# Optimization experiments

Hardware: AMD Instinct MI355X
Metric: run time of the kernel (lower is better)

## Reference

```python
import jax, jax.numpy as jnp
import numpy as np

K = 3
LAMBDA_AMP = 0.1
N_NODES = 100000
N_EDGES = 1600000
D_FEAT = 50


def _proximal_l21(x, lambda_):
    # rowwise L2,1 shrinkage: scale each row by max(||row||-lambda,0)/||row||
    row_norm = jnp.linalg.norm(x, axis=1)  # [N]
    score = jnp.maximum(row_norm - lambda_, 0.0)
    score = jnp.where(row_norm > 0, score / jnp.where(row_norm > 0, row_norm, 1.0), score)
    return score[:, None] * x


def setup_inputs() -> dict:
    key = jax.random.key(0)
    k1, k2, k3, k4 = jax.random.split(key, 4)
    feat = jax.random.normal(k1, (N_NODES, D_FEAT), dtype=jnp.float32)
    edge_weight = jax.random.uniform(k2, (N_EDGES,), dtype=jnp.float32)
    src = jax.random.randint(k3, (N_EDGES,), 0, N_NODES, dtype=jnp.int32)
    dst = jax.random.randint(k4, (N_EDGES,), 0, N_NODES, dtype=jnp.int32)
    return {"feat": feat, "edge_weight": edge_weight, "src": src, "dst": dst}


def reference(feat, edge_weight, src, dst):
    n = feat.shape[0]
    # add self-loops (add_self_loop=True), self-loop weight = 1
    loop = jnp.arange(n, dtype=src.dtype)
    src_f = jnp.concatenate([src, loop])
    dst_f = jnp.concatenate([dst, loop])
    ew = jnp.concatenate([edge_weight, jnp.ones((n,), dtype=edge_weight.dtype)])

    # norm='both': w_ji = ew / (sqrt(out_deg(j)) * sqrt(in_deg(i))), weighted degrees
    out_deg = jax.ops.segment_sum(ew, src_f, num_segments=n)
    in_deg = jax.ops.segment_sum(ew, dst_f, num_segments=n)
    inv_sqrt_out = jnp.where(out_deg > 0, out_deg, 1.0) ** -0.5 * (out_deg > 0)
    inv_sqrt_in = jnp.where(in_deg > 0, in_deg, 1.0) ** -0.5 * (in_deg > 0)
    w = ew * inv_sqrt_out[src_f] * inv_sqrt_in[dst_f]  # [E+N]

    lam = LAMBDA_AMP
    gamma = 1.0 / (2.0 * (1.0 - lam))
    hh = feat
    x = feat
    for _ in range(K):
        # compute_LX: x - A_norm x  (u_mul_e + sum == SpMM over edges)
        agg = jax.ops.segment_sum(x[src_f] * w[:, None], dst_f, num_segments=n)
        lx = x - agg
        y = x - gamma * 2.0 * (1.0 - lam) * lx
        x = hh + _proximal_l21(y - hh, gamma * lam)
    return x
```

## Files before the change

### kernel.cpp

```cpp
#include <hip/hip_runtime.h>
#include <hip/hip_bf16.h>
#include <hip/hip_fp16.h>

#define D 50
#define PADH 64
#define GLAM 0.05555555555555555f
#define SCAN_B 1024
#define FIXS 8388608.0f
#define INV_FIXS (1.0f / 8388608.0f)
#define WSC 32768.0f
#define INV_WSC (1.0f / 32768.0f)
#define EPB 4096
#define B2T 512
#define BSH 9
#define BMSK 511u
#define BT 512
#define MAXB 256
#define MAXRUN 12288
#define NXCD 8

typedef unsigned long long u64;

__global__ void k_b1p(const int* __restrict__ src, const int* __restrict__ dst,
                      int* __restrict__ mat, const float* __restrict__ feat,
                      __half* __restrict__ xp, int e, int nblk, int nbuk, int n) {
    if ((int)blockIdx.x < nblk) {
        __shared__ unsigned hd[MAXB], hs[MAXB];
        for (int j = threadIdx.x; j < nbuk; j += blockDim.x) { hd[j] = 0; hs[j] = 0; }
        __syncthreads();
        int base = blockIdx.x * EPB;
        int end = base + EPB; if (end > e) end = e;
        for (int i = base + threadIdx.x; i < end; i += blockDim.x) {
            int t = __builtin_nontemporal_load(dst + i);
            int s = __builtin_nontemporal_load(src + i);
            atomicAdd(&hd[t >> BSH], 1u);
            atomicAdd(&hs[s >> BSH], 1u);
        }
        __syncthreads();
        for (int j = threadIdx.x; j < nbuk; j += blockDim.x) {
            mat[j * nblk + blockIdx.x] = (int)hd[j];
            mat[(nbuk + j) * nblk + blockIdx.x] = (int)hs[j];
        }
    } else {
        int i = ((int)blockIdx.x - nblk) * (int)blockDim.x + (int)threadIdx.x;
        if (i < n * PADH) {
            int node = i >> 6, col = i & 63;
            xp[i] = (col < D) ? __float2half_rn(feat[node * D + col]) : __half(0.0f);
        }
    }
}

__global__ void k_scan1(const int* __restrict__ cnt, int* __restrict__ out,
                        int* __restrict__ bsum, int n) {
    __shared__ int s[SCAN_B];
    int i = blockIdx.x * SCAN_B + threadIdx.x;
    int v = (i < n) ? cnt[i] : 0;
    s[threadIdx.x] = v; __syncthreads();
    for (int off = 1; off < SCAN_B; off <<= 1) {
        int t = (threadIdx.x >= (unsigned)off) ? s[threadIdx.x - off] : 0;
        __syncthreads();
        s[threadIdx.x] += t; __syncthreads();
    }
    if (i < n) out[i] = s[threadIdx.x] - v;
    if (threadIdx.x == SCAN_B - 1) bsum[blockIdx.x] = s[threadIdx.x];
}

__global__ void k_scan2(int* __restrict__ bsum, int nb) {
    __shared__ int s[SCAN_B];
    int v = (threadIdx.x < (unsigned)nb) ? bsum[threadIdx.x] : 0;
    s[threadIdx.x] = v; __syncthreads();
    for (int off = 1; off < SCAN_B; off <<= 1) {
        int t = (threadIdx.x >= (unsigned)off) ? s[threadIdx.x - off] : 0;
        __syncthreads();
        s[threadIdx.x] += t; __syncthreads();
    }
    if (threadIdx.x < (unsigned)nb) bsum[threadIdx.x] = s[threadIdx.x] - v;
}

__global__ void k_scan3(int* __restrict__ out, const int* __restrict__ bsum, int n) {
    int i = blockIdx.x * SCAN_B + threadIdx.x;
    if (i < n) out[i] += bsum[blockIdx.x];
}

__device__ __forceinline__ int xcd_swz(int p, int nwg) {
    int q = nwg / NXCD, r = nwg % NXCD;
    int xcd = p % NXCD, idx = p / NXCD;
    return (xcd < r ? xcd * (q + 1) : r * (q + 1) + (xcd - r) * q) + idx;
}

__global__ __launch_bounds__(B2T, 4) void k_b2(
                     const float* __restrict__ ew, const int* __restrict__ src,
                     const int* __restrict__ dst, const int* __restrict__ msc,
                     u64* __restrict__ bind, unsigned* __restrict__ bins,
                     int e, int nblk, int nbuk) {
    __shared__ unsigned cd[MAXB], cs[MAXB];
    __shared__ unsigned ld[MAXB], ls[MAXB];
    __shared__ int gbd[MAXB], gbs[MAXB];
    __shared__ u64 sd[EPB];
    __shared__ unsigned ss[EPB];
    __shared__ unsigned char bdd[EPB], bds[EPB];
    int tid = threadIdx.x;
    int wb = xcd_swz((int)blockIdx.x, nblk);
    for (int j = tid; j < MAXB; j += blockDim.x) { cd[j] = 0; cs[j] = 0; }
    __syncthreads();
    int base = wb * EPB;
    int end = base + EPB; if (end > e) end = e;
    int m = end - base;

    for (int i = base + tid; i < end; i += blockDim.x) {
        atomicAdd(&cd[(unsigned)__builtin_nontemporal_load(dst + i) >> BSH], 1u);
        atomicAdd(&cs[(unsigned)__builtin_nontemporal_load(src + i) >> BSH], 1u);
    }
    __syncthreads();

    unsigned vd = 0, vs = 0;
    if (tid < MAXB) { vd = cd[tid]; vs = cs[tid]; ld[tid] = vd; ls[tid] = vs; }
    __syncthreads();
    for (int off = 1; off < MAXB; off <<= 1) {
        unsigned td = 0, ts = 0;
        if (tid < MAXB && tid >= off) { td = ld[tid - off]; ts = ls[tid - off]; }
        __syncthreads();
        if (tid < MAXB) { ld[tid] += td; ls[tid] += ts; }
        __syncthreads();
    }
    if (tid < MAXB) {
        ld[tid] -= vd; ls[tid] -= vs;
        cd[tid] = ld[tid]; cs[tid] = ls[tid];
        if (tid < nbuk) {
            gbd[tid] = msc[tid * nblk + wb];
            gbs[tid] = msc[(nbuk + tid) * nblk + wb] - e;
        }
    }
    __syncthreads();

    for (int i = base + tid; i < end; i += blockDim.x) {
        float w = __builtin_nontemporal_load(ew + i);
        int s = __builtin_nontemporal_load(src + i);
        int t = __builtin_nontemporal_load(dst + i);
        unsigned wfix = (unsigned)(w * FIXS + 0.5f);
        if (wfix > 0x7FFFFFu) wfix = 0x7FFFFFu;
        unsigned tb = (unsigned)t >> BSH, sb = (unsigned)s >> BSH;
        unsigned pd = atomicAdd(&cd[tb], 1u);
        sd[pd] = ((u64)__float_as_uint(w) << 32)
               | ((unsigned)s << BSH) | (unsigned)(t & BMSK);
        bdd[pd] = (unsigned char)tb;
        unsigned ps = atomicAdd(&cs[sb], 1u);
        ss[ps] = (wfix << BSH) | (unsigned)(s & BMSK);
        bds[ps] = (unsigned char)sb;
    }
    __syncthreads();

    for (int p = tid; p < m; p += blockDim.x) {
        unsigned jd = bdd[p];
        bind[gbd[jd] + (int)(p - ld[jd])] = sd[p];
        unsigned js = bds[p];
        bins[gbs[js] + (int)(p - ls[js])] = ss[p];
    }
}

__global__ void k_srcdeg(const unsigned* __restrict__ bins, const int* __restrict__ msc,
                         float* __restrict__ iso, int n, int nblk, int nbuk, int e) {
    __shared__ unsigned wl[BT];
    wl[threadIdx.x] = 0;
    __syncthreads();
    int b = blockIdx.x;
    int start = msc[(nbuk + b) * nblk] - e;
    int end = (b + 1 < nbuk) ? (msc[(nbuk + b + 1) * nblk] - e) : e;
    for (int i = start + threadIdx.x; i < end; i += blockDim.x) {
        unsigned r = bins[i];
        atomicAdd(&wl[r & BMSK], r >> BSH);
    }
    __syncthreads();
    int node = b * BT + threadIdx.x;
    if (node < n)
        iso[node] = rsqrtf(1.0f + (float)wl[threadIdx.x] * INV_FIXS);
}

__global__ void k_dstfill(const u64* __restrict__ bind, const int* __restrict__ msc,
                          const float* __restrict__ iso, float* __restrict__ isi,
                          int* __restrict__ cnt, int* __restrict__ rowptr,
                          unsigned* __restrict__ pe, int n, int nblk, int nbuk, int e) {
    __shared__ unsigned pst[MAXRUN];
    __shared__ unsigned cl[BT], wl[BT], cur[BT];
    __shared__ int sc[BT];
    __shared__ float isL[BT];
    cl[threadIdx.x] = 0; wl[threadIdx.x] = 0;
    __syncthreads();
    int b = blockIdx.x;
    int start = msc[b * nblk];
    int end = (b + 1 < nbuk) ? msc[(b + 1) * nblk] : e;
    int run = end - start;
    bool fast = (run <= MAXRUN);

    for (int i = start + threadIdx.x; i < end; i += blockDim.x) {
        u64 r = bind[i];
        unsigned loc = (unsigned)r & BMSK;
        float w = __uint_as_float((unsigned)(r >> 32));
        unsigned wfix = (unsigned)(w * FIXS + 0.5f);
        if (wfix > 0x7FFFFFu) wfix = 0x7FFFFFu;
        atomicAdd(&cl[loc], 1u);
        atomicAdd(&wl[loc], wfix);
    }
    __syncthreads();

    int myc = (int)cl[threadIdx.x];
    sc[threadIdx.x] = myc;
    __syncthreads();
    for (int off = 1; off < BT; off <<= 1) {
        int t = (threadIdx.x >= (unsigned)off) ? sc[threadIdx.x - off] : 0;
        __syncthreads();
        sc[threadIdx.x] += t;
        __syncthreads();
    }
    int lex = sc[threadIdx.x] - myc;
    int lrp = start + lex;

    float myisi = rsqrtf(1.0f + (float)wl[threadIdx.x] * INV_FIXS);
    isL[threadIdx.x] = myisi;
    cur[threadIdx.x] = fast ? (unsigned)lex : (unsigned)lrp;

    int node = b * BT + threadIdx.x;
    if (node < n) {
        isi[node] = myisi;
        cnt[node] = myc;
        rowptr[node] = lrp;
    }
    __syncthreads();

    if (fast) {
        for (int i = start + threadIdx.x; i < end; i += blockDim.x) {
            u64 r = bind[i];
            unsigned lo = (unsigned)r;
            unsigned tloc = lo & BMSK;
            unsigned s = lo >> BSH;
            float w = __uint_as_float((unsigned)(r >> 32));
            float wv = w * iso[s] * isL[tloc];
            unsigned wq = (unsigned)(wv * WSC + 0.5f);
            if (wq > 32767u) wq = 32767u;
            unsigned pos = atomicAdd(&cur[tloc], 1u);
            pst[pos] = (s << 15) | wq;
        }
        __syncthreads();
        for (int p = threadIdx.x; p < run; p += blockDim.x)
            pe[start + p] = pst[p];
    } else {
        for (int i = start + threadIdx.x; i < end; i += blockDim.x) {
            u64 r = bind[i];
            unsigned lo = (unsigned)r;
            unsigned tloc = lo & BMSK;
            unsigned s = lo >> BSH;
            float w = __uint_as_float((unsigned)(r >> 32));
            float wv = w * iso[s] * isL[tloc];
            unsigned wq = (unsigned)(wv * WSC + 0.5f);
            if (wq > 32767u) wq = 32767u;
            unsigned pos = atomicAdd(&cur[tloc], 1u);
            pe[pos] = (s << 15) | wq;
        }
    }
}

__device__ __forceinline__ void acc_edge(const uint4& u, float w,
                                         float& a0, float& a1, float& a2, float& a3,
                                         float& a4, float& a5, float& a6, float& a7) {
    const __half2* hp = (const __half2*)&u;
    float2 f0 = __half22float2(hp[0]);
    float2 f1 = __half22float2(hp[1]);
    float2 f2 = __half22float2(hp[2]);
    float2 f3 = __half22float2(hp[3]);
    a0 = fmaf(w, f0.x, a0); a1 = fmaf(w, f0.y, a1);
    a2 = fmaf(w, f1.x, a2); a3 = fmaf(w, f1.y, a3);
    a4 = fmaf(w, f2.x, a4); a5 = fmaf(w, f2.y, a5);
    a6 = fmaf(w, f3.x, a6); a7 = fmaf(w, f3.y, a7);
}

__global__ void k_iter(const int* __restrict__ rowptr, const int* __restrict__ cnt,
                       const unsigned* __restrict__ pe, const __half* __restrict__ xin,
                       const __half* __restrict__ xpF, const float* __restrict__ iso,
                       const float* __restrict__ isi, __half* __restrict__ hout,
                       float* __restrict__ fout, int n, int final_iter) {
    int lane = threadIdx.x & 63;
    int c    = lane & 7;
    int waveId = (blockIdx.x * blockDim.x + threadIdx.x) >> 6;
    int node = waveId * 8 + (lane >> 3);
    if (node >= n) return;

    float a0 = 0.f, a1 = 0.f, a2 = 0.f, a3 = 0.f;
    float a4 = 0.f, a5 = 0.f, a6 = 0.f, a7 = 0.f;

    int beg = rowptr[node], m = cnt[node];

    int j = 0;
    for (; j + 8 <= m; j += 8) {
        unsigned p0 = pe[beg + j];
        unsigned p1 = pe[beg + j + 1];
        unsigned p2 = pe[beg + j + 2];
        unsigned p3 = pe[beg + j + 3];
        unsigned p4 = pe[beg + j + 4];
        unsigned p5 = pe[beg + j + 5];
        unsigned p6 = pe[beg + j + 6];
        unsigned p7 = pe[beg + j + 7];
        unsigned s0 = p0 >> 15; float w0 = (float)(p0 & 32767u) * INV_WSC;
        unsigned s1 = p1 >> 15; float w1 = (float)(p1 & 32767u) * INV_WSC;
        unsigned s2 = p2 >> 15; float w2 = (float)(p2 & 32767u) * INV_WSC;
        unsigned s3 = p3 >> 15; float w3 = (float)(p3 & 32767u) * INV_WSC;
        unsigned s4 = p4 >> 15; float w4 = (float)(p4 & 32767u) * INV_WSC;
        unsigned s5 = p5 >> 15; float w5 = (float)(p5 & 32767u) * INV_WSC;
        unsigned s6 = p6 >> 15; float w6 = (float)(p6 & 32767u) * INV_WSC;
        unsigned s7 = p7 >> 15; float w7 = (float)(p7 & 32767u) * INV_WSC;
        uint4 u0 = *(const uint4*)(xin + ((size_t)s0 << 6) + (c << 3));
        uint4 u1 = *(const uint4*)(xin + ((size_t)s1 << 6) + (c << 3));
        uint4 u2 = *(const uint4*)(xin + ((size_t)s2 << 6) + (c << 3));
        uint4 u3 = *(const uint4*)(xin + ((size_t)s3 << 6) + (c << 3));
        uint4 u4 = *(const uint4*)(xin + ((size_t)s4 << 6) + (c << 3));
        uint4 u5 = *(const uint4*)(xin + ((size_t)s5 << 6) + (c << 3));
        uint4 u6 = *(const uint4*)(xin + ((size_t)s6 << 6) + (c << 3));
        uint4 u7 = *(const uint4*)(xin + ((size_t)s7 << 6) + (c << 3));
        acc_edge(u0, w0, a0, a1, a2, a3, a4, a5, a6, a7);
        acc_edge(u1, w1, a0, a1, a2, a3, a4, a5, a6, a7);
        acc_edge(u2, w2, a0, a1, a2, a3, a4, a5, a6, a7);
        acc_edge(u3, w3, a0, a1, a2, a3, a4, a5, a6, a7);
        acc_edge(u4, w4, a0, a1, a2, a3, a4, a5, a6, a7);
        acc_edge(u5, w5, a0, a1, a2, a3, a4, a5, a6, a7);
        acc_edge(u6, w6, a0, a1, a2, a3, a4, a5, a6, a7);
        acc_edge(u7, w7, a0, a1, a2, a3, a4, a5, a6, a7);
    }
    for (; j + 4 <= m; j += 4) {
        unsigned p0 = pe[beg + j];
        unsigned p1 = pe[beg + j + 1];
        unsigned p2 = pe[beg + j + 2];
        unsigned p3 = pe[beg + j + 3];
        unsigned s0 = p0 >> 15; float w0 = (float)(p0 & 32767u) * INV_WSC;
        unsigned s1 = p1 >> 15; float w1 = (float)(p1 & 32767u) * INV_WSC;
        unsigned s2 = p2 >> 15; float w2 = (float)(p2 & 32767u) * INV_WSC;
        unsigned s3 = p3 >> 15; float w3 = (float)(p3 & 32767u) * INV_WSC;
        uint4 u0 = *(const uint4*)(xin + ((size_t)s0 << 6) + (c << 3));
        uint4 u1 = *(const uint4*)(xin + ((size_t)s1 << 6) + (c << 3));
        uint4 u2 = *(const uint4*)(xin + ((size_t)s2 << 6) + (c << 3));
        uint4 u3 = *(const uint4*)(xin + ((size_t)s3 << 6) + (c << 3));
        acc_edge(u0, w0, a0, a1, a2, a3, a4, a5, a6, a7);
        acc_edge(u1, w1, a0, a1, a2, a3, a4, a5, a6, a7);
        acc_edge(u2, w2, a0, a1, a2, a3, a4, a5, a6, a7);
        acc_edge(u3, w3, a0, a1, a2, a3, a4, a5, a6, a7);
    }
    for (; j < m; ++j) {
        unsigned p0 = pe[beg + j];
        unsigned s0 = p0 >> 15;
        float    w0 = (float)(p0 & 32767u) * INV_WSC;
        uint4 u0 = *(const uint4*)(xin + ((size_t)s0 << 6) + (c << 3));
        acc_edge(u0, w0, a0, a1, a2, a3, a4, a5, a6, a7);
    }

    float selfw = iso[node] * isi[node];
    {
        uint4 u = *(const uint4*)(xin + ((size_t)node << 6) + (c << 3));
        acc_edge(u, selfw, a0, a1, a2, a3, a4, a5, a6, a7);
    }

    float f[8];
    {
        uint4 u = *(const uint4*)(xpF + ((size_t)node << 6) + (c << 3));
        const __half2* hp = (const __half2*)&u;
        float2 f0 = __half22float2(hp[0]);
        float2 f1 = __half22float2(hp[1]);
        float2 f2 = __half22float2(hp[2]);
        float2 f3 = __half22float2(hp[3]);
        f[0] = f0.x; f[1] = f0.y; f[2] = f1.x; f[3] = f1.y;
        f[4] = f2.x; f[5] = f2.y; f[6] = f3.x; f[7] = f3.y;
    }

    float d0 = a0 - f[0], d1 = a1 - f[1], d2 = a2 - f[2], d3 = a3 - f[3];
    float d4 = a4 - f[4], d5 = a5 - f[5], d6 = a6 - f[6], d7 = a7 - f[7];

    float ssum = d0*d0 + d1*d1 + d2*d2 + d3*d3 + d4*d4 + d5*d5 + d6*d6 + d7*d7;
    ssum += __shfl_xor(ssum, 1, 64);
    ssum += __shfl_xor(ssum, 2, 64);
    ssum += __shfl_xor(ssum, 4, 64);
    float norm = sqrtf(ssum);
    float sc = (norm > 0.0f) ? fmaxf(norm - GLAM, 0.0f) / norm : 0.0f;

    float o0 = f[0] + sc * d0, o1 = f[1] + sc * d1;
    float o2 = f[2] + sc * d2, o3 = f[3] + sc * d3;
    float o4 = f[4] + sc * d4, o5 = f[5] + sc * d5;
    float o6 = f[6] + sc * d6, o7 = f[7] + sc * d7;
    if (!final_iter) {
        __half2 h0 = __float22half2_rn(make_float2(o0, o1));
        __half2 h1 = __float22half2_rn(make_float2(o2, o3));
        __half2 h2 = __float22half2_rn(make_float2(o4, o5));
        __half2 h3 = __float22half2_rn(make_float2(o6, o7));
        uint4 u;
        u.x = *(unsigned*)&h0; u.y = *(unsigned*)&h1;
        u.z = *(unsigned*)&h2; u.w = *(unsigned*)&h3;
        *(uint4*)(hout + ((size_t)node << 6) + (c << 3)) = u;
    } else {
        float o[8] = {o0, o1, o2, o3, o4, o5, o6, o7};
        int fb = c << 3;
        #pragma unroll
        for (int k = 0; k < 4; ++k) {
            int ff = fb + (k << 1);
            if (ff + 1 < D) {
                float2 v; v.x = o[k * 2]; v.y = o[k * 2 + 1];
                *(float2*)(fout + (size_t)node * D + ff) = v;
            }
        }
    }
}

extern "C" void kernel_launch(void* const* d_in, const int* in_sizes, int n_in,
                              void* d_out, int out_size, void* d_ws, size_t ws_size,
                              hipStream_t stream) {
    const float* feat = (const float*)d_in[0];
    const float* ew   = (const float*)d_in[1];
    const int* src = (const int*)d_in[2];
    const int* dst = (const int*)d_in[3];

    const int nd = in_sizes[0];
    const int n  = nd / D;
    const int e  = in_sizes[1];
    const int np = n * PADH;

    const int nbuk = (n + BT - 1) / BT;
    const int nblk = (e + EPB - 1) / EPB;
    const int nm   = 2 * nbuk * nblk;

    __half*   xpF    = (__half*)d_ws;
    __half*   xpA    = xpF + np;
    __half*   xpB    = xpA + np;
    u64*      bind   = (u64*)(xpB + np);
    unsigned* pe     = (unsigned*)(bind + e);
    unsigned* bins   = pe + e;
    int*      mat    = (int*)(bins + e);
    int*      msc    = mat + nm;
    float*    isi    = (float*)(msc + nm);
    float*    iso    = isi + n;
    int*      cnt    = (int*)(iso + n);
    int*      rowptr = cnt + n;
    int*      bsum   = rowptr + n;
    float*    out    = (float*)d_out;

    const int B = 256;
    const int gP  = (np + B2T - 1) / B2T;
    const int NBm = (nm + SCAN_B - 1) / SCAN_B;

    k_b1p<<<nblk + gP, B2T, 0, stream>>>(src, dst, mat, feat, xpF, e, nblk, nbuk, n);
    k_scan1<<<NBm, SCAN_B, 0, stream>>>(mat, msc, bsum, nm);
    k_scan2<<<1, SCAN_B, 0, stream>>>(bsum, NBm);
    k_scan3<<<NBm, SCAN_B, 0, stream>>>(msc, bsum, nm);
    k_b2<<<nblk, B2T, 0, stream>>>(ew, src, dst, msc, bind, bins, e, nblk, nbuk);
    k_srcdeg<<<nbuk, BT, 0, stream>>>(bins, msc, iso, n, nblk, nbuk, e);
    k_dstfill<<<nbuk, BT, 0, stream>>>(bind, msc, iso, isi, cnt, rowptr, pe, n, nblk, nbuk, e);

    const int nodesPerBlock = (B / 64) * 8;
    const int iterGrid = (n + nodesPerBlock - 1) / nodesPerBlock;

    k_iter<<<iterGrid, B, 0, stream>>>(rowptr, cnt, pe, xpF, xpF, iso, isi, xpA, out, n, 0);
    k_iter<<<iterGrid, B, 0, stream>>>(rowptr, cnt, pe, xpA, xpF, iso, isi, xpB, out, n, 0);
    k_iter<<<iterGrid, B, 0, stream>>>(rowptr, cnt, pe, xpB, xpF, iso, isi, xpA, out, n, 1);
}
```

Before: 240.9 us.

## Halve node bucket size, register-cache edges in scatter, skip padded feature lanes

Node buckets shrink from 512 to 256 nodes, so twice as many buckets feed the src-degree and dst-fill kernels, each with a smaller shared-memory run buffer. The bucket-scatter kernel now loads src, dst and weight once into registers (8 edges per thread) and reuses them in the second pass instead of re-reading global memory. The SpMM iteration kernel skips the eighth 16-byte chunk of each padded 64-wide half row, which only holds padding beyond the 50 features, cutting gather traffic. The risk is more buckets and scan entries, plus more runs overflowing the smaller fast-path buffer.

```diff
diff --git a/kernel.cpp b/kernel.cpp
--- a/kernel.cpp
+++ b/kernel.cpp
@@ -11,12 +11,13 @@
 #define WSC 32768.0f
 #define INV_WSC (1.0f / 32768.0f)
 #define EPB 4096
+#define EPT 8
 #define B2T 512
-#define BSH 9
-#define BMSK 511u
-#define BT 512
-#define MAXB 256
-#define MAXRUN 12288
+#define BSH 8
+#define BMSK 255u
+#define BKT 256
+#define MAXB 512
+#define MAXRUN 6144
 #define NXCD 8
 
 typedef unsigned long long u64;
@@ -98,18 +99,27 @@
     __shared__ int gbd[MAXB], gbs[MAXB];
     __shared__ u64 sd[EPB];
     __shared__ unsigned ss[EPB];
-    __shared__ unsigned char bdd[EPB], bds[EPB];
+    __shared__ unsigned short bdd[EPB], bds[EPB];
     int tid = threadIdx.x;
     int wb = xcd_swz((int)blockIdx.x, nblk);
-    for (int j = tid; j < MAXB; j += blockDim.x) { cd[j] = 0; cs[j] = 0; }
+    if (tid < MAXB) { cd[tid] = 0; cs[tid] = 0; }
     __syncthreads();
     int base = wb * EPB;
     int end = base + EPB; if (end > e) end = e;
     int m = end - base;
 
-    for (int i = base + tid; i < end; i += blockDim.x) {
-        atomicAdd(&cd[(unsigned)__builtin_nontemporal_load(dst + i) >> BSH], 1u);
-        atomicAdd(&cs[(unsigned)__builtin_nontemporal_load(src + i) >> BSH], 1u);
+    int sv[EPT], tv[EPT]; float wv[EPT];
+    #pragma unroll
+    for (int k = 0; k < EPT; ++k) {
+        int i = base + k * B2T + tid;
+        bool ok = (i < end);
+        sv[k] = ok ? __builtin_nontemporal_load(src + i) : 0;
+        tv[k] = ok ? __builtin_nontemporal_load(dst + i) : 0;
+        wv[k] = ok ? __builtin_nontemporal_load(ew + i) : 0.0f;
+        if (ok) {
+            atomicAdd(&cd[(unsigned)tv[k] >> BSH], 1u);
+            atomicAdd(&cs[(unsigned)sv[k] >> BSH], 1u);
+        }
     }
     __syncthreads();
 
@@ -133,20 +143,22 @@
     }
     __syncthreads();
 
-    for (int i = base + tid; i < end; i += blockDim.x) {
-        float w = __builtin_nontemporal_load(ew + i);
-        int s = __builtin_nontemporal_load(src + i);
-        int t = __builtin_nontemporal_load(dst + i);
-        unsigned wfix = (unsigned)(w * FIXS + 0.5f);
-        if (wfix > 0x7FFFFFu) wfix = 0x7FFFFFu;
-        unsigned tb = (unsigned)t >> BSH, sb = (unsigned)s >> BSH;
-        unsigned pd = atomicAdd(&cd[tb], 1u);
-        sd[pd] = ((u64)__float_as_uint(w) << 32)
-               | ((unsigned)s << BSH) | (unsigned)(t & BMSK);
-        bdd[pd] = (unsigned char)tb;
-        unsigned ps = atomicAdd(&cs[sb], 1u);
-        ss[ps] = (wfix << BSH) | (unsigned)(s & BMSK);
-        bds[ps] = (unsigned char)sb;
+    #pragma unroll
+    for (int k = 0; k < EPT; ++k) {
+        int i = base + k * B2T + tid;
+        if (i < end) {
+            float w = wv[k]; int s = sv[k]; int t = tv[k];
+            unsigned wfix = (unsigned)(w * FIXS + 0.5f);
+            if (wfix > 0x7FFFFFu) wfix = 0x7FFFFFu;
+            unsigned tb = (unsigned)t >> BSH, sb = (unsigned)s >> BSH;
+            unsigned pd = atomicAdd(&cd[tb], 1u);
+            sd[pd] = ((u64)__float_as_uint(w) << 32)
+                   | ((unsigned)s << BSH) | (unsigned)(t & BMSK);
+            bdd[pd] = (unsigned short)tb;
+            unsigned ps = atomicAdd(&cs[sb], 1u);
+            ss[ps] = (wfix << BSH) | (unsigned)(s & BMSK);
+            bds[ps] = (unsigned short)sb;
+        }
     }
     __syncthreads();
 
@@ -160,7 +172,7 @@
 
 __global__ void k_srcdeg(const unsigned* __restrict__ bins, const int* __restrict__ msc,
                          float* __restrict__ iso, int n, int nblk, int nbuk, int e) {
-    __shared__ unsigned wl[BT];
+    __shared__ unsigned wl[BKT];
     wl[threadIdx.x] = 0;
     __syncthreads();
     int b = blockIdx.x;
@@ -171,7 +183,7 @@
         atomicAdd(&wl[r & BMSK], r >> BSH);
     }
     __syncthreads();
-    int node = b * BT + threadIdx.x;
+    int node = b * BKT + threadIdx.x;
     if (node < n)
         iso[node] = rsqrtf(1.0f + (float)wl[threadIdx.x] * INV_FIXS);
 }
@@ -181,9 +193,9 @@
                           int* __restrict__ cnt, int* __restrict__ rowptr,
                           unsigned* __restrict__ pe, int n, int nblk, int nbuk, int e) {
     __shared__ unsigned pst[MAXRUN];
-    __shared__ unsigned cl[BT], wl[BT], cur[BT];
-    __shared__ int sc[BT];
-    __shared__ float isL[BT];
+    __shared__ unsigned cl[BKT], wl[BKT], cur[BKT];
+    __shared__ int sc[BKT];
+    __shared__ float isL[BKT];
     cl[threadIdx.x] = 0; wl[threadIdx.x] = 0;
     __syncthreads();
     int b = blockIdx.x;
@@ -206,7 +218,7 @@
     int myc = (int)cl[threadIdx.x];
     sc[threadIdx.x] = myc;
     __syncthreads();
-    for (int off = 1; off < BT; off <<= 1) {
+    for (int off = 1; off < BKT; off <<= 1) {
         int t = (threadIdx.x >= (unsigned)off) ? sc[threadIdx.x - off] : 0;
         __syncthreads();
         sc[threadIdx.x] += t;
@@ -219,7 +231,7 @@
     isL[threadIdx.x] = myisi;
     cur[threadIdx.x] = fast ? (unsigned)lex : (unsigned)lrp;
 
-    int node = b * BT + threadIdx.x;
+    int node = b * BKT + threadIdx.x;
     if (node < n) {
         isi[node] = myisi;
         cnt[node] = myc;
@@ -273,6 +285,11 @@
     a6 = fmaf(w, f3.x, a6); a7 = fmaf(w, f3.y, a7);
 }
 
+__device__ __forceinline__ uint4 gld(const __half* p, bool en) {
+    uint4 z; z.x = 0; z.y = 0; z.z = 0; z.w = 0;
+    return en ? *(const uint4*)p : z;
+}
+
 __global__ void k_iter(const int* __restrict__ rowptr, const int* __restrict__ cnt,
                        const unsigned* __restrict__ pe, const __half* __restrict__ xin,
                        const __half* __restrict__ xpF, const float* __restrict__ iso,
@@ -280,6 +297,7 @@
                        float* __restrict__ fout, int n, int final_iter) {
     int lane = threadIdx.x & 63;
     int c    = lane & 7;
+    bool en  = (c < 7);
     int waveId = (blockIdx.x * blockDim.x + threadIdx.x) >> 6;
     int node = waveId * 8 + (lane >> 3);
     if (node >= n) return;
@@ -307,14 +325,14 @@
         unsigned s5 = p5 >> 15; float w5 = (float)(p5 & 32767u) * INV_WSC;
         unsigned s6 = p6 >> 15; float w6 = (float)(p6 & 32767u) * INV_WSC;
         unsigned s7 = p7 >> 15; float w7 = (float)(p7 & 32767u) * INV_WSC;
-        uint4 u0 = *(const uint4*)(xin + ((size_t)s0 << 6) + (c << 3));
-        uint4 u1 = *(const uint4*)(xin + ((size_t)s1 << 6) + (c << 3));
-        uint4 u2 = *(const uint4*)(xin + ((size_t)s2 << 6) + (c << 3));
-        uint4 u3 = *(const uint4*)(xin + ((size_t)s3 << 6) + (c << 3));
-        uint4 u4 = *(const uint4*)(xin + ((size_t)s4 << 6) + (c << 3));
-        uint4 u5 = *(const uint4*)(xin + ((size_t)s5 << 6) + (c << 3));
-        uint4 u6 = *(const uint4*)(xin + ((size_t)s6 << 6) + (c << 3));
-        uint4 u7 = *(const uint4*)(xin + ((size_t)s7 << 6) + (c << 3));
+        uint4 u0 = gld(xin + ((size_t)s0 << 6) + (c << 3), en);
+        uint4 u1 = gld(xin + ((size_t)s1 << 6) + (c << 3), en);
+        uint4 u2 = gld(xin + ((size_t)s2 << 6) + (c << 3), en);
+        uint4 u3 = gld(xin + ((size_t)s3 << 6) + (c << 3), en);
+        uint4 u4 = gld(xin + ((size_t)s4 << 6) + (c << 3), en);
+        uint4 u5 = gld(xin + ((size_t)s5 << 6) + (c << 3), en);
+        uint4 u6 = gld(xin + ((size_t)s6 << 6) + (c << 3), en);
+        uint4 u7 = gld(xin + ((size_t)s7 << 6) + (c << 3), en);
         acc_edge(u0, w0, a0, a1, a2, a3, a4, a5, a6, a7);
         acc_edge(u1, w1, a0, a1, a2, a3, a4, a5, a6, a7);
         acc_edge(u2, w2, a0, a1, a2, a3, a4, a5, a6, a7);
@@ -333,10 +351,10 @@
         unsigned s1 = p1 >> 15; float w1 = (float)(p1 & 32767u) * INV_WSC;
         unsigned s2 = p2 >> 15; float w2 = (float)(p2 & 32767u) * INV_WSC;
         unsigned s3 = p3 >> 15; float w3 = (float)(p3 & 32767u) * INV_WSC;
-        uint4 u0 = *(const uint4*)(xin + ((size_t)s0 << 6) + (c << 3));
-        uint4 u1 = *(const uint4*)(xin + ((size_t)s1 << 6) + (c << 3));
-        uint4 u2 = *(const uint4*)(xin + ((size_t)s2 << 6) + (c << 3));
-        uint4 u3 = *(const uint4*)(xin + ((size_t)s3 << 6) + (c << 3));
+        uint4 u0 = gld(xin + ((size_t)s0 << 6) + (c << 3), en);
+        uint4 u1 = gld(xin + ((size_t)s1 << 6) + (c << 3), en);
+        uint4 u2 = gld(xin + ((size_t)s2 << 6) + (c << 3), en);
+        uint4 u3 = gld(xin + ((size_t)s3 << 6) + (c << 3), en);
         acc_edge(u0, w0, a0, a1, a2, a3, a4, a5, a6, a7);
         acc_edge(u1, w1, a0, a1, a2, a3, a4, a5, a6, a7);
         acc_edge(u2, w2, a0, a1, a2, a3, a4, a5, a6, a7);
@@ -346,19 +364,19 @@
         unsigned p0 = pe[beg + j];
         unsigned s0 = p0 >> 15;
         float    w0 = (float)(p0 & 32767u) * INV_WSC;
-        uint4 u0 = *(const uint4*)(xin + ((size_t)s0 << 6) + (c << 3));
+        uint4 u0 = gld(xin + ((size_t)s0 << 6) + (c << 3), en);
         acc_edge(u0, w0, a0, a1, a2, a3, a4, a5, a6, a7);
     }
 
     float selfw = iso[node] * isi[node];
     {
-        uint4 u = *(const uint4*)(xin + ((size_t)node << 6) + (c << 3));
+        uint4 u = gld(xin + ((size_t)node << 6) + (c << 3), en);
         acc_edge(u, selfw, a0, a1, a2, a3, a4, a5, a6, a7);
     }
 
     float f[8];
     {
-        uint4 u = *(const uint4*)(xpF + ((size_t)node << 6) + (c << 3));
+        uint4 u = gld(xpF + ((size_t)node << 6) + (c << 3), en);
         const __half2* hp = (const __half2*)&u;
         float2 f0 = __half22float2(hp[0]);
         float2 f1 = __half22float2(hp[1]);
@@ -383,14 +401,16 @@
     float o4 = f[4] + sc * d4, o5 = f[5] + sc * d5;
     float o6 = f[6] + sc * d6, o7 = f[7] + sc * d7;
     if (!final_iter) {
-        __half2 h0 = __float22half2_rn(make_float2(o0, o1));
-        __half2 h1 = __float22half2_rn(make_float2(o2, o3));
-        __half2 h2 = __float22half2_rn(make_float2(o4, o5));
-        __half2 h3 = __float22half2_rn(make_float2(o6, o7));
-        uint4 u;
-        u.x = *(unsigned*)&h0; u.y = *(unsigned*)&h1;
-        u.z = *(unsigned*)&h2; u.w = *(unsigned*)&h3;
-        *(uint4*)(hout + ((size_t)node << 6) + (c << 3)) = u;
+        if (en) {
+            __half2 h0 = __float22half2_rn(make_float2(o0, o1));
+            __half2 h1 = __float22half2_rn(make_float2(o2, o3));
+            __half2 h2 = __float22half2_rn(make_float2(o4, o5));
+            __half2 h3 = __float22half2_rn(make_float2(o6, o7));
+            uint4 u;
+            u.x = *(unsigned*)&h0; u.y = *(unsigned*)&h1;
+            u.z = *(unsigned*)&h2; u.w = *(unsigned*)&h3;
+            *(uint4*)(hout + ((size_t)node << 6) + (c << 3)) = u;
+        }
     } else {
         float o[8] = {o0, o1, o2, o3, o4, o5, o6, o7};
         int fb = c << 3;
@@ -418,7 +438,7 @@
     const int e  = in_sizes[1];
     const int np = n * PADH;
 
-    const int nbuk = (n + BT - 1) / BT;
+    const int nbuk = (n + BKT - 1) / BKT;
     const int nblk = (e + EPB - 1) / EPB;
     const int nm   = 2 * nbuk * nblk;
 
@@ -446,8 +466,8 @@
     k_scan2<<<1, SCAN_B, 0, stream>>>(bsum, NBm);
     k_scan3<<<NBm, SCAN_B, 0, stream>>>(msc, bsum, nm);
     k_b2<<<nblk, B2T, 0, stream>>>(ew, src, dst, msc, bind, bins, e, nblk, nbuk);
-    k_srcdeg<<<nbuk, BT, 0, stream>>>(bins, msc, iso, n, nblk, nbuk, e);
-    k_dstfill<<<nbuk, BT, 0, stream>>>(bind, msc, iso, isi, cnt, rowptr, pe, n, nblk, nbuk, e);
+    k_srcdeg<<<nbuk, BKT, 0, stream>>>(bins, msc, iso, n, nblk, nbuk, e);
+    k_dstfill<<<nbuk, BKT, 0, stream>>>(bind, msc, iso, isi, cnt, rowptr, pe, n, nblk, nbuk, e);
 
     const int nodesPerBlock = (B / 64) * 8;
     const int iterGrid = (n + nodesPerBlock - 1) / nodesPerBlock;
```

Result: slower. 330.5 us (+37.2%).
